# Kernel tuning notes

Measured on AMD Instinct MI355X. Metric: run time of the kernel, lower is better.

## Reference

```python
import jax, jax.numpy as jnp
import numpy as np

N_DST = 50000
N_SRC = 50000
E = 800000
D = 128
R = 3
H_SEM = 128
NEG_SLOPE = 0.2  # DGL GATConv default


def setup_inputs() -> dict:
    key = jax.random.key(0)
    ks = jax.random.split(key, 40)
    s = 1.0 / np.sqrt(D)
    inp = {
        'dst_feat': jax.random.normal(ks[0], (N_DST, D), jnp.float32),
        'src_feat0': jax.random.normal(ks[1], (N_SRC, D), jnp.float32),
        'src_feat1': jax.random.normal(ks[2], (N_SRC, D), jnp.float32),
        'src_feat2': jax.random.normal(ks[3], (N_SRC, D), jnp.float32),
        'sem_W1': jax.random.normal(ks[4], (D, H_SEM), jnp.float32) * s,
        'sem_b1': jnp.zeros((H_SEM,), jnp.float32),
        'sem_W2': jax.random.normal(ks[5], (H_SEM, 1), jnp.float32) * (1.0 / np.sqrt(H_SEM)),
    }
    for r in range(R):
        inp[f'Wg{r}'] = jax.random.normal(ks[6 + r], (D, D), jnp.float32) * s
        inp[f'al{r}'] = jax.random.normal(ks[9 + r], (D,), jnp.float32) * s
        inp[f'ar{r}'] = jax.random.normal(ks[12 + r], (D,), jnp.float32) * s
        inp[f'bg{r}'] = jnp.zeros((D,), jnp.float32)
        inp[f'src_idx{r}'] = jax.random.randint(ks[15 + r], (E,), 0, N_SRC, jnp.int32)
        inp[f'dst_idx{r}'] = jax.random.randint(ks[18 + r], (E,), 0, N_DST, jnp.int32)
    return inp


def _gat(fs, fd, W, al, ar, b, sidx, didx):
    # DGL GATConv, num_heads=1, bipartite, eval mode (no dropout)
    hs = fs @ W                    # [Ns, D]
    hd = fd @ W                    # [Nd, D]
    el = hs @ al                   # [Ns]
    er = hd @ ar                   # [Nd]
    e = jax.nn.leaky_relu(el[sidx] + er[didx], NEG_SLOPE)  # [E]
    # edge softmax over incoming edges of each dst node
    m = jax.ops.segment_max(e, didx, num_segments=N_DST)
    a = jnp.exp(e - m[didx])
    z = jax.ops.segment_sum(a, didx, num_segments=N_DST)
    alpha = a / z[didx]            # [E]
    out = jax.ops.segment_sum(hs[sidx] * alpha[:, None], didx, num_segments=N_DST)
    return jax.nn.elu(out + b)     # [Nd, D]


def reference(dst_feat, src_feat0, src_feat1, src_feat2,
              Wg0, Wg1, Wg2, al0, al1, al2, ar0, ar1, ar2, bg0, bg1, bg2,
              sem_W1, sem_b1, sem_W2,
              src_idx0, src_idx1, src_idx2, dst_idx0, dst_idx1, dst_idx2):
    z0 = _gat(src_feat0, dst_feat, Wg0, al0, ar0, bg0, src_idx0, dst_idx0)
    z1 = _gat(src_feat1, dst_feat, Wg1, al1, ar1, bg1, src_idx1, dst_idx1)
    z2 = _gat(src_feat2, dst_feat, Wg2, al2, ar2, bg2, src_idx2, dst_idx2)
    z_m = jnp.stack([z0, z1, z2], axis=1)            # [N, R, D]
    h = jnp.tanh(z_m @ sem_W1 + sem_b1) @ sem_W2     # [N, R, 1]
    w = h.mean(axis=0)                               # [R, 1]
    a_w = jax.nn.softmax(w, axis=0)                  # [R, 1]
    z = (z_m * a_w[None, :, :]).sum(axis=1)          # [N, D]
    att_mp = a_w.squeeze()                           # [R]
    return (z, att_mp)
```

## Files before the change

kernel.cpp:

```cpp
#include <hip/hip_runtime.h>
#include <math.h>

#define D_DIM 128
#define N_DST 50000
#define N_SRC 50000
#define NE    800000
#define NEG_SLOPE 0.2f

#define NB        196
#define CAP       4608
#define CHUNK     8192
#define NBLK_REL  98
#define GEMM_BLKS 391
#define GEMM_GRID (3 * GEMM_BLKS)

typedef unsigned short ushort_t;
using f32x4  = __attribute__((ext_vector_type(4))) float;
using bf16x8 = __attribute__((ext_vector_type(8))) short;

__device__ __forceinline__ ushort_t f2bf(float x) {
    unsigned u = __float_as_uint(x);
    unsigned r = (u + 0x7fffu + ((u >> 16) & 1u)) >> 16;
    return (ushort_t)r;
}
__device__ __forceinline__ float bf2f(ushort_t b) {
    return __uint_as_float(((unsigned)b) << 16);
}
__device__ __forceinline__ float bflo(unsigned u) { return __uint_as_float(u << 16); }
__device__ __forceinline__ float bfhi(unsigned u) { return __uint_as_float(u & 0xffff0000u); }
__device__ __forceinline__ float tanh_fast(float x) {
    float e = __expf(2.f * x);
    return 1.f - 2.f / (e + 1.f);
}

__global__ __launch_bounds__(256) void vecprep_kernel(
        const float* __restrict__ Wg0, const float* __restrict__ Wg1,
        const float* __restrict__ Wg2,
        const float* __restrict__ ar0, const float* __restrict__ ar1,
        const float* __restrict__ ar2,
        const float* __restrict__ W1,
        float* __restrict__ wv, ushort_t* __restrict__ Wt_g,
        ushort_t* __restrict__ WgT_hi, ushort_t* __restrict__ WgT_lo) {
    int bx = blockIdx.x, tid = threadIdx.x;
    if (bx < 3) {
        if (tid < 128) {
            const float* W  = bx == 0 ? Wg0 : (bx == 1 ? Wg1 : Wg2);
            const float* ar = bx == 0 ? ar0 : (bx == 1 ? ar1 : ar2);
            float sar = 0.f;
            for (int j = 0; j < D_DIM; j++) sar = fmaf(W[tid * D_DIM + j], ar[j], sar);
            wv[bx * D_DIM + tid] = sar;
        }
    } else if (bx < 67) {
        int idx = (bx - 3) * 256 + tid;
        int k = idx >> 7, n = idx & 127;
        Wt_g[n * 128 + k] = f2bf(W1[idx]);
    } else {
        int q = bx - 67;
        int rel = q >> 6;
        int idx = (q & 63) * 256 + tid;
        const float* W = rel == 0 ? Wg0 : (rel == 1 ? Wg1 : Wg2);
        int k = idx >> 7, n = idx & 127;
        float v = W[idx];
        ushort_t hi = f2bf(v);
        float lo = v - bf2f(hi);
        WgT_hi[rel * 16384 + n * 128 + k] = hi;
        WgT_lo[rel * 16384 + n * 128 + k] = f2bf(lo);
    }
}

__global__ __launch_bounds__(256) void bucket_scatter_kernel(
        const int* __restrict__ d0, const int* __restrict__ d1, const int* __restrict__ d2,
        const int* __restrict__ s0, const int* __restrict__ s1, const int* __restrict__ s2,
        int* __restrict__ bucketCur, int2* __restrict__ pairs) {
    __shared__ int cnt[NB], base[NB], cur[NB];
    int bx = blockIdx.x;
    int r = bx / NBLK_REL, blk = bx % NBLK_REL;
    const int* dd = r == 0 ? d0 : (r == 1 ? d1 : d2);
    const int* ss = r == 0 ? s0 : (r == 1 ? s1 : s2);
    int tid = threadIdx.x;
    if (tid < NB) { cnt[tid] = 0; cur[tid] = 0; }
    __syncthreads();
    int e0 = blk * CHUNK, e1 = min(e0 + CHUNK, NE);
    for (int e = e0 + tid; e < e1; e += 256) atomicAdd(&cnt[dd[e] >> 8], 1);
    __syncthreads();
    if (tid < NB) base[tid] = cnt[tid] ? atomicAdd(&bucketCur[r * NB + tid], cnt[tid]) : 0;
    __syncthreads();
    for (int e = e0 + tid; e < e1; e += 256) {
        int d = dd[e], b = d >> 8;
        int rank = atomicAdd(&cur[b], 1);
        pairs[(size_t)(r * NB + b) * CAP + base[b] + rank] = make_int2(ss[e], d);
    }
}

__global__ __launch_bounds__(256) void csr_kernel(
        const int2* __restrict__ pairs, const int* __restrict__ bucketCur,
        int* __restrict__ offs, int* __restrict__ cnts, int* __restrict__ perm) {
    __shared__ int hist[256], sc[256], cur[256];
    int bx = blockIdx.x;
    int r = bx / NB, b = bx % NB;
    int tid = threadIdx.x;
    int nE = bucketCur[r * NB + b];
    size_t region = (size_t)(r * NB + b) * CAP;
    const int2* pr = pairs + region;
    hist[tid] = 0;
    __syncthreads();
    for (int i = tid; i < nE; i += 256) atomicAdd(&hist[pr[i].y & 255], 1);
    __syncthreads();
    int v = hist[tid];
    sc[tid] = v;
    __syncthreads();
    for (int off = 1; off < 256; off <<= 1) {
        int t = tid >= off ? sc[tid - off] : 0;
        __syncthreads();
        sc[tid] += t;
        __syncthreads();
    }
    int excl = sc[tid] - v;
    int dstg = b * 256 + tid;
    if (dstg < N_DST) { offs[r * N_DST + dstg] = (int)region + excl; cnts[r * N_DST + dstg] = v; }
    cur[tid] = excl;
    __syncthreads();
    int* pm = perm + region;
    for (int i = tid; i < nE; i += 256) {
        int2 p = pr[i];
        int rank = atomicAdd(&cur[p.y & 255], 1);
        pm[rank] = p.x;
    }
}

__global__ __launch_bounds__(256) void gemm_er_kernel(
        const float* __restrict__ A0, const float* __restrict__ A1, const float* __restrict__ A2,
        const ushort_t* __restrict__ WgT_hi, const ushort_t* __restrict__ WgT_lo,
        const float* __restrict__ al0, const float* __restrict__ al1, const float* __restrict__ al2,
        const float* __restrict__ dstf, const float* __restrict__ wv,
        ushort_t* __restrict__ hs, float* __restrict__ elv) {
    int bx = blockIdx.x;
    if (bx >= GEMM_GRID) {
        int eb   = bx - GEMM_GRID;
        int wave = threadIdx.x >> 6, lane = threadIdx.x & 63;
        int row  = eb * 4 + wave;
        const float* mr = dstf + (size_t)row * D_DIM;
        float m0 = mr[lane], m1 = mr[lane + 64];
        #pragma unroll
        for (int r = 0; r < 3; r++) {
            float p = fmaf(m0, wv[r * 128 + lane], m1 * wv[r * 128 + lane + 64]);
            #pragma unroll
            for (int off = 32; off > 0; off >>= 1) p += __shfl_down(p, off);
            if (lane == 0) elv[(3 + r) * N_DST + row] = p;
        }
        return;
    }
    __shared__ ushort_t wls[4][2560];
    int rel = bx / GEMM_BLKS, blk = bx % GEMM_BLKS;
    const float* A  = rel == 0 ? A0 : (rel == 1 ? A1 : A2);
    const float* al = rel == 0 ? al0 : (rel == 1 ? al1 : al2);
    const ushort_t* Bh = WgT_hi + rel * 16384;
    const ushort_t* Bl = WgT_lo + rel * 16384;
    ushort_t* C = hs + (size_t)rel * N_SRC * 128;

    int w = threadIdx.x >> 6, lane = threadIdx.x & 63;
    int quad = lane >> 4, l15 = lane & 15;
    int row0 = blk * 128 + w * 32;
    ushort_t* Ah = wls[w];
    ushort_t* Al = wls[w] + 1280;

    f32x4 acc[2][8] = {};
    #pragma unroll
    for (int kc = 0; kc < 4; kc++) {
        #pragma unroll
        for (int j = 0; j < 4; j++) {
            int pp = lane + j * 64;
            int r = pp >> 3, c4 = (pp & 7) * 4;
            int gr = row0 + r; if (gr > N_SRC - 1) gr = N_SRC - 1;
            float4 f = *(const float4*)&A[(size_t)gr * 128 + kc * 32 + c4];
            ushort4 h4, l4;
            h4.x = f2bf(f.x); l4.x = (ushort_t)(__float_as_uint(f.x - bf2f(h4.x)) >> 16);
            h4.y = f2bf(f.y); l4.y = (ushort_t)(__float_as_uint(f.y - bf2f(h4.y)) >> 16);
            h4.z = f2bf(f.z); l4.z = (ushort_t)(__float_as_uint(f.z - bf2f(h4.z)) >> 16);
            h4.w = f2bf(f.w); l4.w = (ushort_t)(__float_as_uint(f.w - bf2f(h4.w)) >> 16);
            *(ushort4*)&Ah[r * 40 + c4] = h4;
            *(ushort4*)&Al[r * 40 + c4] = l4;
        }
        __asm__ __volatile__("" ::: "memory");
        bf16x8 ah[2], alo[2];
        #pragma unroll
        for (int t = 0; t < 2; t++) {
            ah[t]  = *(const bf16x8*)&Ah[(l15 + t * 16) * 40 + quad * 8];
            alo[t] = *(const bf16x8*)&Al[(l15 + t * 16) * 40 + quad * 8];
        }
        int koff = kc * 32 + quad * 8;
        #pragma unroll
        for (int nt = 0; nt < 8; nt++) {
            bf16x8 bh = *(const bf16x8*)&Bh[(nt * 16 + l15) * 128 + koff];
            bf16x8 bl = *(const bf16x8*)&Bl[(nt * 16 + l15) * 128 + koff];
            #pragma unroll
            for (int t = 0; t < 2; t++) {
                acc[t][nt] = __builtin_amdgcn_mfma_f32_16x16x32_bf16(ah[t],  bh, acc[t][nt], 0, 0, 0);
                acc[t][nt] = __builtin_amdgcn_mfma_f32_16x16x32_bf16(alo[t], bh, acc[t][nt], 0, 0, 0);
                acc[t][nt] = __builtin_amdgcn_mfma_f32_16x16x32_bf16(ah[t],  bl, acc[t][nt], 0, 0, 0);
            }
        }
        __asm__ __volatile__("" ::: "memory");
    }

    float alv[8];
    #pragma unroll
    for (int nt = 0; nt < 8; nt++) alv[nt] = al[nt * 16 + l15];
    #pragma unroll
    for (int t = 0; t < 2; t++) {
        float part[4] = {0.f, 0.f, 0.f, 0.f};
        #pragma unroll
        for (int nt = 0; nt < 8; nt++)
            #pragma unroll
            for (int i = 0; i < 4; i++)
                part[i] = fmaf(acc[t][nt][i], alv[nt], part[i]);
        #pragma unroll
        for (int msk = 1; msk < 16; msk <<= 1)
            #pragma unroll
            for (int i = 0; i < 4; i++) part[i] += __shfl_xor(part[i], msk);
        if (l15 == 0) {
            #pragma unroll
            for (int i = 0; i < 4; i++) {
                int gr = row0 + t * 16 + quad * 4 + i;
                if (gr < N_SRC) elv[rel * N_DST + gr] = part[i];
            }
        }
    }

    ushort_t* Csh = wls[w];
    #pragma unroll
    for (int h = 0; h < 2; h++) {
        __asm__ __volatile__("" ::: "memory");
        #pragma unroll
        for (int t = 0; t < 2; t++)
            #pragma unroll
            for (int ntl = 0; ntl < 4; ntl++) {
                int nt = h * 4 + ntl;
                #pragma unroll
                for (int i = 0; i < 4; i++)
                    Csh[(t * 16 + quad * 4 + i) * 72 + ntl * 16 + l15] = f2bf(acc[t][nt][i]);
            }
        __asm__ __volatile__("" ::: "memory");
        int r2 = lane >> 1, cb = (lane & 1) * 32;
        int gr = row0 + r2;
        if (gr < N_SRC) {
            ushort_t* dst = C + (size_t)gr * 128 + h * 64 + cb;
            #pragma unroll
            for (int k2 = 0; k2 < 4; k2++) {
                uint4 v = *(const uint4*)&Csh[r2 * 72 + cb + k2 * 8];
                *(uint4*)(dst + k2 * 8) = v;
            }
        }
    }
}

__global__ __launch_bounds__(256) void aggregate_kernel(
        const ushort_t* __restrict__ hs, const float* __restrict__ elv,
        const int* __restrict__ perm, const int* __restrict__ offs,
        const int* __restrict__ cnts,
        const float* __restrict__ bg0, const float* __restrict__ bg1,
        const float* __restrict__ bg2, float* __restrict__ zm) {
    __shared__ int2 ew[4][128];
    int wave = threadIdx.x >> 6, lane = threadIdx.x & 63;
    int bx  = blockIdx.x;
    int rel = bx / 12500;
    int b   = (bx % 12500) * 4 + wave;
    const float* el  = elv + rel * N_DST;
    float erb = elv[(3 + rel) * N_DST + b];
    const float* bg = rel == 0 ? bg0 : (rel == 1 ? bg1 : bg2);
    const ushort_t* hsr = hs + (size_t)rel * N_SRC * 128;
    int o0 = offs[rel * N_DST + b], deg = cnts[rel * N_DST + b];
    float* zout = zm + ((size_t)b * 3 + rel) * 128;

    if (deg <= 128) {
        int i0 = lane, i1 = lane + 64;
        int s0 = 0, s1 = 0;
        float x0 = -INFINITY, x1 = -INFINITY;
        if (i0 < deg) { s0 = perm[o0 + i0]; float x = el[s0] + erb; x0 = x >= 0.f ? x : NEG_SLOPE * x; }
        if (i1 < deg) { s1 = perm[o0 + i1]; float x = el[s1] + erb; x1 = x >= 0.f ? x : NEG_SLOPE * x; }
        float m = fmaxf(x0, x1);
        #pragma unroll
        for (int msk = 1; msk < 64; msk <<= 1) m = fmaxf(m, __shfl_xor(m, msk));
        float e0 = (i0 < deg) ? __expf(x0 - m) : 0.f;
        float e1 = (i1 < deg) ? __expf(x1 - m) : 0.f;
        float lsum = e0 + e1;
        #pragma unroll
        for (int msk = 1; msk < 64; msk <<= 1) lsum += __shfl_xor(lsum, msk);
        float invz = deg > 0 ? 1.f / lsum : 0.f;

        ew[wave][i0] = make_int2(s0 * 256, __float_as_int(e0 * invz));
        ew[wave][i1] = make_int2(s1 * 256, __float_as_int(e1 * invz));
        __asm__ __volatile__("" ::: "memory");

        int degp = (deg + 7) & ~7;
        const char* base = (const char*)hsr;
        int half = lane >> 5;
        int col8 = (lane & 31) * 8;
        float2 a01 = {0.f, 0.f}, a23 = {0.f, 0.f};
        for (int j = 0; j < degp; j += 8) {
            int2 pA = ew[wave][j + half];
            int2 pB = ew[wave][j + 2 + half];
            int2 pC = ew[wave][j + 4 + half];
            int2 pD = ew[wave][j + 6 + half];
            uint2 hA = *(const uint2*)(base + (unsigned)(pA.x + col8));
            uint2 hB = *(const uint2*)(base + (unsigned)(pB.x + col8));
            uint2 hC = *(const uint2*)(base + (unsigned)(pC.x + col8));
            uint2 hD = *(const uint2*)(base + (unsigned)(pD.x + col8));
            float eA = __int_as_float(pA.y), eB = __int_as_float(pB.y);
            float eC = __int_as_float(pC.y), eD = __int_as_float(pD.y);
            a01.x = fmaf(eA, bflo(hA.x), a01.x); a01.y = fmaf(eA, bfhi(hA.x), a01.y);
            a23.x = fmaf(eA, bflo(hA.y), a23.x); a23.y = fmaf(eA, bfhi(hA.y), a23.y);
            a01.x = fmaf(eB, bflo(hB.x), a01.x); a01.y = fmaf(eB, bfhi(hB.x), a01.y);
            a23.x = fmaf(eB, bflo(hB.y), a23.x); a23.y = fmaf(eB, bfhi(hB.y), a23.y);
            a01.x = fmaf(eC, bflo(hC.x), a01.x); a01.y = fmaf(eC, bfhi(hC.x), a01.y);
            a23.x = fmaf(eC, bflo(hC.y), a23.x); a23.y = fmaf(eC, bfhi(hC.y), a23.y);
            a01.x = fmaf(eD, bflo(hD.x), a01.x); a01.y = fmaf(eD, bfhi(hD.x), a01.y);
            a23.x = fmaf(eD, bflo(hD.y), a23.x); a23.y = fmaf(eD, bfhi(hD.y), a23.y);
        }
        a01.x += __shfl_xor(a01.x, 32);
        a01.y += __shfl_xor(a01.y, 32);
        a23.x += __shfl_xor(a23.x, 32);
        a23.y += __shfl_xor(a23.y, 32);
        if (half == 0) {
            int col4 = (lane & 31) * 4;
            float4 bgv = *(const float4*)&bg[col4];
            float4 z;
            z.x = a01.x + bgv.x;
            z.y = a01.y + bgv.y;
            z.z = a23.x + bgv.z;
            z.w = a23.y + bgv.w;
            z.x = z.x > 0.f ? z.x : expm1f(z.x);
            z.y = z.y > 0.f ? z.y : expm1f(z.y);
            z.z = z.z > 0.f ? z.z : expm1f(z.z);
            z.w = z.w > 0.f ? z.w : expm1f(z.w);
            *(float4*)&zout[col4] = z;
        }
    } else {
        float lmax = -INFINITY;
        for (int i = lane; i < deg; i += 64) {
            int s = perm[o0 + i];
            float x = el[s] + erb;
            x = x >= 0.f ? x : NEG_SLOPE * x;
            lmax = fmaxf(lmax, x);
        }
        #pragma unroll
        for (int msk = 1; msk < 64; msk <<= 1) lmax = fmaxf(lmax, __shfl_xor(lmax, msk));
        float lsum = 0.f;
        for (int i = lane; i < deg; i += 64) {
            int s = perm[o0 + i];
            float x = el[s] + erb;
            x = x >= 0.f ? x : NEG_SLOPE * x;
            lsum += __expf(x - lmax);
        }
        #pragma unroll
        for (int msk = 1; msk < 64; msk <<= 1) lsum += __shfl_xor(lsum, msk);
        float invz = 1.f / lsum;
        float c0 = 0.f, c1 = 0.f;
        int col2 = lane * 2;
        for (int j = 0; j < deg; j++) {
            int s = perm[o0 + j];
            float x = el[s] + erb;
            x = x >= 0.f ? x : NEG_SLOPE * x;
            float e_ = __expf(x - lmax) * invz;
            unsigned hv = *(const unsigned*)(hsr + (size_t)s * 128 + col2);
            c0 = fmaf(e_, bflo(hv), c0);
            c1 = fmaf(e_, bfhi(hv), c1);
        }
        float2 z;
        z.x = c0 + bg[col2];
        z.y = c1 + bg[col2 + 1];
        z.x = z.x > 0.f ? z.x : expm1f(z.x);
        z.y = z.y > 0.f ? z.y : expm1f(z.y);
        *(float2*)&zout[col2] = z;
    }
}

__global__ __launch_bounds__(256) void semantic_kernel(
        const float* __restrict__ zm, const ushort_t* __restrict__ Wt_g,
        const float* __restrict__ b1, const float* __restrict__ W2,
        float* __restrict__ w_sum) {
    __shared__ ushort_t Wt[128 * 136];
    __shared__ float hsum[3];
    const int NROWS = N_DST * 3;
    int tid = threadIdx.x;
    if (tid < 3) hsum[tid] = 0.f;

    #pragma unroll
    for (int i = 0; i < 8; i++) {
        int c = i * 256 + tid;
        int n = c >> 4, c16 = c & 15;
        uint4 t = *(const uint4*)(Wt_g + n * 128 + c16 * 8);
        *(uint4*)&Wt[n * 136 + c16 * 8] = t;
    }
    __syncthreads();

    int w    = tid >> 6, lane = tid & 63;
    int quad = lane >> 4, l15 = lane & 15;
    long row0 = (long)blockIdx.x * 64 + w * 16;
    long rA = row0 + l15; if (rA > NROWS - 1) rA = NROWS - 1;

    f32x4 acc[8] = {};
    #pragma unroll
    for (int kc = 0; kc < 4; kc++) {
        int k0 = kc * 32 + quad * 8;
        const float* src = zm + (size_t)rA * 128 + k0;
        float4 f0 = *(const float4*)src;
        float4 f1 = *(const float4*)(src + 4);
        bf16x8 a;
        a[0] = (short)f2bf(f0.x); a[1] = (short)f2bf(f0.y);
        a[2] = (short)f2bf(f0.z); a[3] = (short)f2bf(f0.w);
        a[4] = (short)f2bf(f1.x); a[5] = (short)f2bf(f1.y);
        a[6] = (short)f2bf(f1.z); a[7] = (short)f2bf(f1.w);
        #pragma unroll
        for (int nt = 0; nt < 8; nt++) {
            int n = nt * 16 + l15;
            bf16x8 bfr = *(const bf16x8*)&Wt[n * 136 + k0];
            acc[nt] = __builtin_amdgcn_mfma_f32_16x16x32_bf16(a, bfr, acc[nt], 0, 0, 0);
        }
    }

    float part[4] = {0.f, 0.f, 0.f, 0.f};
    #pragma unroll
    for (int nt = 0; nt < 8; nt++) {
        int n = nt * 16 + l15;
        float bb = b1[n], ww = W2[n];
        #pragma unroll
        for (int i = 0; i < 4; i++) {
            float t = tanh_fast(acc[nt][i] + bb);
            part[i] = fmaf(t, ww, part[i]);
        }
    }
    #pragma unroll
    for (int msk = 1; msk < 16; msk <<= 1)
        #pragma unroll
        for (int i = 0; i < 4; i++) part[i] += __shfl_xor(part[i], msk);
    if (l15 == 0) {
        #pragma unroll
        for (int i = 0; i < 4; i++) {
            long R = row0 + quad * 4 + i;
            if (R < NROWS) atomicAdd(&hsum[(int)(R % 3)], part[i]);
        }
    }
    __syncthreads();
    if (tid < 3) atomicAdd(&w_sum[tid], hsum[tid]);
}

__global__ void combine_kernel(const float* __restrict__ zm, const float* __restrict__ w_sum,
                               float* __restrict__ out, float* __restrict__ out_att) {
    float w0 = w_sum[0] * (1.f / (float)N_DST);
    float w1 = w_sum[1] * (1.f / (float)N_DST);
    float w2 = w_sum[2] * (1.f / (float)N_DST);
    float m = fmaxf(w0, fmaxf(w1, w2));
    float e0 = __expf(w0 - m), e1 = __expf(w1 - m), e2 = __expf(w2 - m);
    float s = 1.f / (e0 + e1 + e2);
    float a0 = e0 * s, a1 = e1 * s, a2 = e2 * s;
    if (blockIdx.x == 0 && threadIdx.x < 3)
        out_att[threadIdx.x] = threadIdx.x == 0 ? a0 : (threadIdx.x == 1 ? a1 : a2);
    int id4 = blockIdx.x * 256 + threadIdx.x;
    int n  = id4 >> 5;
    int d4 = (id4 & 31) * 4;
    const float4 z0 = *(const float4*)&zm[((size_t)n * 3 + 0) * 128 + d4];
    const float4 z1 = *(const float4*)&zm[((size_t)n * 3 + 1) * 128 + d4];
    const float4 z2 = *(const float4*)&zm[((size_t)n * 3 + 2) * 128 + d4];
    float4 o;
    o.x = a0 * z0.x + a1 * z1.x + a2 * z2.x;
    o.y = a0 * z0.y + a1 * z1.y + a2 * z2.y;
    o.z = a0 * z0.z + a1 * z1.z + a2 * z2.z;
    o.w = a0 * z0.w + a1 * z1.w + a2 * z2.w;
    *(float4*)&out[(size_t)n * 128 + d4] = o;
}

extern "C" void kernel_launch(void* const* d_in, const int* in_sizes, int n_in,
                              void* d_out, int out_size, void* d_ws, size_t ws_size,
                              hipStream_t stream) {
    const float* dstf   = (const float*)d_in[0];
    const float* src0   = (const float*)d_in[1];
    const float* src1   = (const float*)d_in[2];
    const float* src2   = (const float*)d_in[3];
    const float* sem_W1 = (const float*)d_in[4];
    const float* sem_b1 = (const float*)d_in[5];
    const float* sem_W2 = (const float*)d_in[6];
    const float* Wg[3]  = {(const float*)d_in[7],  (const float*)d_in[13], (const float*)d_in[19]};
    const float* al[3]  = {(const float*)d_in[8],  (const float*)d_in[14], (const float*)d_in[20]};
    const float* ar[3]  = {(const float*)d_in[9],  (const float*)d_in[15], (const float*)d_in[21]};
    const float* bg[3]  = {(const float*)d_in[10], (const float*)d_in[16], (const float*)d_in[22]};
    const int*  sidx[3] = {(const int*)d_in[11], (const int*)d_in[17], (const int*)d_in[23]};
    const int*  didx[3] = {(const int*)d_in[12], (const int*)d_in[18], (const int*)d_in[24]};
    float* out = (float*)d_out;

    char* p = (char*)d_ws;
    auto alloc = [&](size_t bytes) -> char* {
        char* q = p; p += (bytes + 255) & ~(size_t)255; return q;
    };
    float*    zm   = (float*)alloc((size_t)N_DST * 3 * 128 * 4);
    ushort_t* hs   = (ushort_t*)alloc((size_t)3 * N_SRC * 128 * 2);
    float*    elv  = (float*)alloc((size_t)6 * N_DST * 4);
    float*    wv   = (float*)alloc((size_t)3 * 128 * 4);
    ushort_t* Wt_g   = (ushort_t*)alloc((size_t)128 * 128 * 2);
    ushort_t* WgT_hi = (ushort_t*)alloc((size_t)3 * 16384 * 2);
    ushort_t* WgT_lo = (ushort_t*)alloc((size_t)3 * 16384 * 2);
    int* cnts = (int*)alloc((size_t)3 * N_DST * 4);
    int* offs = (int*)alloc((size_t)3 * N_DST * 4);
    int* perm = (int*)alloc((size_t)3 * NB * CAP * 4);
    int* zero = (int*)alloc((size_t)(3 * NB + 8) * 4);
    int*   bucketCur = zero;
    float* wsum      = (float*)(zero + 3 * NB);
    int2* pairs = (int2*)zm;

    hipMemsetAsync(zero, 0, (size_t)(3 * NB + 8) * 4, stream);

    vecprep_kernel<<<259, 256, 0, stream>>>(Wg[0], Wg[1], Wg[2], ar[0], ar[1], ar[2],
                                            sem_W1, wv, Wt_g, WgT_hi, WgT_lo);
    bucket_scatter_kernel<<<3 * NBLK_REL, 256, 0, stream>>>(didx[0], didx[1], didx[2],
                                                            sidx[0], sidx[1], sidx[2],
                                                            bucketCur, pairs);
    csr_kernel<<<3 * NB, 256, 0, stream>>>(pairs, bucketCur, offs, cnts, perm);
    gemm_er_kernel<<<GEMM_GRID + 12500, 256, 0, stream>>>(src0, src1, src2,
                                                          WgT_hi, WgT_lo,
                                                          al[0], al[1], al[2],
                                                          dstf, wv, hs, elv);
    aggregate_kernel<<<3 * 12500, 256, 0, stream>>>(hs, elv, perm, offs, cnts,
                                                    bg[0], bg[1], bg[2], zm);
    semantic_kernel<<<(3 * N_DST + 63) / 64, 256, 0, stream>>>(zm, Wt_g, sem_b1, sem_W2, wsum);
    combine_kernel<<<6250, 256, 0, stream>>>(zm, wsum, out, out + (size_t)N_DST * 128);
}
```

Baseline: 485.9 us.

## Register-prefetch GEMM A operands and fold er dot products into GEMM blocks

```diff
diff --git a/kernel.cpp b/kernel.cpp
--- a/kernel.cpp
+++ b/kernel.cpp
@@ -13,6 +13,7 @@
 #define NBLK_REL  98
 #define GEMM_BLKS 391
 #define GEMM_GRID (3 * GEMM_BLKS)
+#define ER_PB     43
 
 typedef unsigned short ushort_t;
 using f32x4  = __attribute__((ext_vector_type(4))) float;
@@ -31,6 +32,16 @@
 __device__ __forceinline__ float tanh_fast(float x) {
     float e = __expf(2.f * x);
     return 1.f - 2.f / (e + 1.f);
+}
+
+__device__ __forceinline__ void cvt8(float4 f0, float4 f1, bf16x8& hi, bf16x8& lo) {
+    float f[8] = {f0.x, f0.y, f0.z, f0.w, f1.x, f1.y, f1.z, f1.w};
+    #pragma unroll
+    for (int i = 0; i < 8; i++) {
+        ushort_t h = f2bf(f[i]);
+        hi[i] = (short)h;
+        lo[i] = (short)(ushort_t)(__float_as_uint(f[i] - bf2f(h)) >> 16);
+    }
 }
 
 __global__ __launch_bounds__(256) void vecprep_kernel(
@@ -134,23 +145,8 @@
         const float* __restrict__ al0, const float* __restrict__ al1, const float* __restrict__ al2,
         const float* __restrict__ dstf, const float* __restrict__ wv,
         ushort_t* __restrict__ hs, float* __restrict__ elv) {
+    __shared__ ushort_t wls[4][2304];
     int bx = blockIdx.x;
-    if (bx >= GEMM_GRID) {
-        int eb   = bx - GEMM_GRID;
-        int wave = threadIdx.x >> 6, lane = threadIdx.x & 63;
-        int row  = eb * 4 + wave;
-        const float* mr = dstf + (size_t)row * D_DIM;
-        float m0 = mr[lane], m1 = mr[lane + 64];
-        #pragma unroll
-        for (int r = 0; r < 3; r++) {
-            float p = fmaf(m0, wv[r * 128 + lane], m1 * wv[r * 128 + lane + 64]);
-            #pragma unroll
-            for (int off = 32; off > 0; off >>= 1) p += __shfl_down(p, off);
-            if (lane == 0) elv[(3 + r) * N_DST + row] = p;
-        }
-        return;
-    }
-    __shared__ ushort_t wls[4][2560];
     int rel = bx / GEMM_BLKS, blk = bx % GEMM_BLKS;
     const float* A  = rel == 0 ? A0 : (rel == 1 ? A1 : A2);
     const float* al = rel == 0 ? al0 : (rel == 1 ? al1 : al2);
@@ -161,46 +157,55 @@
     int w = threadIdx.x >> 6, lane = threadIdx.x & 63;
     int quad = lane >> 4, l15 = lane & 15;
     int row0 = blk * 128 + w * 32;
-    ushort_t* Ah = wls[w];
-    ushort_t* Al = wls[w] + 1280;
+
+    int gr0 = row0 + l15;      if (gr0 > N_SRC - 1) gr0 = N_SRC - 1;
+    int gr1 = row0 + 16 + l15; if (gr1 > N_SRC - 1) gr1 = N_SRC - 1;
+    const float* a0p = A + (size_t)gr0 * 128 + quad * 8;
+    const float* a1p = A + (size_t)gr1 * 128 + quad * 8;
+
+    float4 abuf[2][2][2];
+    abuf[0][0][0] = *(const float4*)(a0p + 0);
+    abuf[0][0][1] = *(const float4*)(a0p + 4);
+    abuf[0][1][0] = *(const float4*)(a1p + 0);
+    abuf[0][1][1] = *(const float4*)(a1p + 4);
 
     f32x4 acc[2][8] = {};
     #pragma unroll
     for (int kc = 0; kc < 4; kc++) {
-        #pragma unroll
-        for (int j = 0; j < 4; j++) {
-            int pp = lane + j * 64;
-            int r = pp >> 3, c4 = (pp & 7) * 4;
-            int gr = row0 + r; if (gr > N_SRC - 1) gr = N_SRC - 1;
-            float4 f = *(const float4*)&A[(size_t)gr * 128 + kc * 32 + c4];
-            ushort4 h4, l4;
-            h4.x = f2bf(f.x); l4.x = (ushort_t)(__float_as_uint(f.x - bf2f(h4.x)) >> 16);
-            h4.y = f2bf(f.y); l4.y = (ushort_t)(__float_as_uint(f.y - bf2f(h4.y)) >> 16);
-            h4.z = f2bf(f.z); l4.z = (ushort_t)(__float_as_uint(f.z - bf2f(h4.z)) >> 16);
-            h4.w = f2bf(f.w); l4.w = (ushort_t)(__float_as_uint(f.w - bf2f(h4.w)) >> 16);
-            *(ushort4*)&Ah[r * 40 + c4] = h4;
-            *(ushort4*)&Al[r * 40 + c4] = l4;
-        }
-        __asm__ __volatile__("" ::: "memory");
+        const int par = kc & 1;
+        if (kc < 3) {
+            int ko = (kc + 1) * 32;
+            abuf[par ^ 1][0][0] = *(const float4*)(a0p + ko);
+            abuf[par ^ 1][0][1] = *(const float4*)(a0p + ko + 4);
+            abuf[par ^ 1][1][0] = *(const float4*)(a1p + ko);
+            abuf[par ^ 1][1][1] = *(const float4*)(a1p + ko + 4);
+        }
         bf16x8 ah[2], alo[2];
         #pragma unroll
-        for (int t = 0; t < 2; t++) {
-            ah[t]  = *(const bf16x8*)&Ah[(l15 + t * 16) * 40 + quad * 8];
-            alo[t] = *(const bf16x8*)&Al[(l15 + t * 16) * 40 + quad * 8];
-        }
+        for (int t = 0; t < 2; t++)
+            cvt8(abuf[par][t][0], abuf[par][t][1], ah[t], alo[t]);
+
         int koff = kc * 32 + quad * 8;
         #pragma unroll
-        for (int nt = 0; nt < 8; nt++) {
-            bf16x8 bh = *(const bf16x8*)&Bh[(nt * 16 + l15) * 128 + koff];
-            bf16x8 bl = *(const bf16x8*)&Bl[(nt * 16 + l15) * 128 + koff];
-            #pragma unroll
-            for (int t = 0; t < 2; t++) {
-                acc[t][nt] = __builtin_amdgcn_mfma_f32_16x16x32_bf16(ah[t],  bh, acc[t][nt], 0, 0, 0);
-                acc[t][nt] = __builtin_amdgcn_mfma_f32_16x16x32_bf16(alo[t], bh, acc[t][nt], 0, 0, 0);
-                acc[t][nt] = __builtin_amdgcn_mfma_f32_16x16x32_bf16(ah[t],  bl, acc[t][nt], 0, 0, 0);
+        for (int h2 = 0; h2 < 2; h2++) {
+            bf16x8 bhv[4], blv[4];
+            #pragma unroll
+            for (int n4 = 0; n4 < 4; n4++) {
+                int nt = h2 * 4 + n4;
+                bhv[n4] = *(const bf16x8*)&Bh[(nt * 16 + l15) * 128 + koff];
+                blv[n4] = *(const bf16x8*)&Bl[(nt * 16 + l15) * 128 + koff];
             }
-        }
-        __asm__ __volatile__("" ::: "memory");
+            #pragma unroll
+            for (int n4 = 0; n4 < 4; n4++) {
+                int nt = h2 * 4 + n4;
+                #pragma unroll
+                for (int t = 0; t < 2; t++) {
+                    acc[t][nt] = __builtin_amdgcn_mfma_f32_16x16x32_bf16(ah[t],  bhv[n4], acc[t][nt], 0, 0, 0);
+                    acc[t][nt] = __builtin_amdgcn_mfma_f32_16x16x32_bf16(alo[t], bhv[n4], acc[t][nt], 0, 0, 0);
+                    acc[t][nt] = __builtin_amdgcn_mfma_f32_16x16x32_bf16(ah[t],  blv[n4], acc[t][nt], 0, 0, 0);
+                }
+            }
+        }
     }
 
     float alv[8];
@@ -249,6 +254,42 @@
             for (int k2 = 0; k2 < 4; k2++) {
                 uint4 v = *(const uint4*)&Csh[r2 * 72 + cb + k2 * 8];
                 *(uint4*)(dst + k2 * 8) = v;
+            }
+        }
+    }
+
+    int base = bx * ER_PB;
+    if (base < N_DST) {
+        int rend = min(base + ER_PB, N_DST);
+        float wl0 = wv[lane],       wh0 = wv[lane + 64];
+        float wl1 = wv[128 + lane], wh1 = wv[128 + lane + 64];
+        float wl2 = wv[256 + lane], wh2 = wv[256 + lane + 64];
+        float m0[11], m1[11];
+        #pragma unroll
+        for (int j = 0; j < 11; j++) {
+            int r = base + w + 4 * j;
+            int rr = r < rend ? r : base;
+            m0[j] = dstf[(size_t)rr * 128 + lane];
+            m1[j] = dstf[(size_t)rr * 128 + lane + 64];
+        }
+        #pragma unroll
+        for (int j = 0; j < 11; j++) {
+            int r = base + w + 4 * j;
+            if (r < rend) {
+                float p0 = fmaf(m0[j], wl0, m1[j] * wh0);
+                float p1 = fmaf(m0[j], wl1, m1[j] * wh1);
+                float p2 = fmaf(m0[j], wl2, m1[j] * wh2);
+                #pragma unroll
+                for (int off = 32; off > 0; off >>= 1) {
+                    p0 += __shfl_down(p0, off);
+                    p1 += __shfl_down(p1, off);
+                    p2 += __shfl_down(p2, off);
+                }
+                if (lane == 0) {
+                    elv[3 * N_DST + r] = p0;
+                    elv[4 * N_DST + r] = p1;
+                    elv[5 * N_DST + r] = p2;
+                }
             }
         }
     }
@@ -515,10 +556,10 @@
                                                             sidx[0], sidx[1], sidx[2],
                                                             bucketCur, pairs);
     csr_kernel<<<3 * NB, 256, 0, stream>>>(pairs, bucketCur, offs, cnts, perm);
-    gemm_er_kernel<<<GEMM_GRID + 12500, 256, 0, stream>>>(src0, src1, src2,
-                                                          WgT_hi, WgT_lo,
-                                                          al[0], al[1], al[2],
-                                                          dstf, wv, hs, elv);
+    gemm_er_kernel<<<GEMM_GRID, 256, 0, stream>>>(src0, src1, src2,
+                                                  WgT_hi, WgT_lo,
+                                                  al[0], al[1], al[2],
+                                                  dstf, wv, hs, elv);
     aggregate_kernel<<<3 * 12500, 256, 0, stream>>>(hs, elv, perm, offs, cnts,
                                                     bg[0], bg[1], bg[2], zm);
     semantic_kernel<<<(3 * N_DST + 63) / 64, 256, 0, stream>>>(zm, Wt_g, sem_b1, sem_W2, wsum);
```

New measurement: 467.1 us. 1.04x faster.
